# Kernel tuning notes

Measured on AMD Instinct MI355X. Metric: run time of the kernel, lower is better.

## Reference

```python
import jax, jax.numpy as jnp
import numpy as np

S, D = 16384, 1024


def setup_inputs() -> dict:
    key = jax.random.key(0)
    ks = jax.random.split(key, 7)
    stdv = 1.0 / np.sqrt(D)
    u = lambda k, shape: jax.random.uniform(k, shape, jnp.float32, -stdv, stdv)
    return {
        "x": jax.random.normal(ks[0], (S, D), jnp.float32),
        "Wq": u(ks[1], (D, D)), "bq": u(ks[2], (D,)),
        "Wk": u(ks[3], (D, D)), "bk": u(ks[4], (D,)),
        "Wv": u(ks[5], (D, D)), "bv": u(ks[6], (D,)),
    }


def reference(x, Wq, bq, Wk, bk, Wv, bv):
    # torch.nn.Linear: y = x @ W^T + b
    q = x @ Wq.T + bq          # [S, D]
    k = x @ Wk.T + bk          # [S, D]
    v = x @ Wv.T + bv          # [S, D]
    d = x.shape[-1]
    # NOTE: faithful to source -- scores are over the FEATURE axis: [D, D]
    scores = jnp.einsum('sd,se->de', q, k) / jnp.sqrt(jnp.float32(d))
    attn = jax.nn.softmax(scores, axis=-1)   # [D, D]
    out = v @ attn                           # [S, D]
    return out, attn
```

## Files before the change

kernel.cpp:

```cpp
#include <hip/hip_runtime.h>
#include <hip/hip_bf16.h>
#include <stdint.h>


#define S_ 16384
#define D_ 1024

typedef _Float16 half8 __attribute__((ext_vector_type(8)));
typedef _Float16 half4 __attribute__((ext_vector_type(4)));
typedef float f32x4 __attribute__((ext_vector_type(4)));

__device__ __forceinline__ void gload_lds16(const _Float16* g, _Float16* l) {
    __builtin_amdgcn_global_load_lds(
        (const __attribute__((address_space(1))) void*)g,
        (__attribute__((address_space(3))) void*)l, 16, 0, 0);
}

#define VM8() do { asm volatile("s_waitcnt vmcnt(8)" ::: "memory"); __builtin_amdgcn_sched_barrier(0); } while (0)
#define VM0() do { asm volatile("s_waitcnt vmcnt(0)" ::: "memory"); __builtin_amdgcn_sched_barrier(0); } while (0)
#define BAR() __builtin_amdgcn_s_barrier()
#define LGKM0() do { asm volatile("s_waitcnt lgkmcnt(0)" ::: "memory"); __builtin_amdgcn_sched_barrier(0); } while (0)
#define LGKM8() do { asm volatile("s_waitcnt lgkmcnt(8)" ::: "memory"); __builtin_amdgcn_sched_barrier(0); } while (0)
#define PRIO1() __builtin_amdgcn_s_setprio(1)
#define PRIO0() __builtin_amdgcn_s_setprio(0)

#define STAGEA(H, KT, NX) do { \
    const _Float16* _s = srcA + (size_t)((H) * 128) * lda + (size_t)(KT) * 64; \
    _Float16* _d = AsS + (NX) * 16384 + ((H) * 128 + 8 * w) * 64; \
    gload_lds16(_s, _d); \
    gload_lds16(_s + (size_t)64 * lda, _d + 4096); \
} while (0)

#define STAGEB(H, KT, NX) do { \
    const _Float16* _s = srcB + (size_t)((H) * 128) * ldb + (size_t)(KT) * 64; \
    _Float16* _d = BsS + (NX) * 16384 + ((H) * 128 + 8 * w) * 64; \
    gload_lds16(_s, _d); \
    gload_lds16(_s + (size_t)64 * ldb, _d + 4096); \
} while (0)

#define READA(PA, QA) do { _Pragma("unroll") \
    for (int fm = 0; fm < 4; ++fm) { \
        af[fm][0] = *(const half8*)((PA) + (((QA) * 128 + fm * 16) << 7) + cx0); \
        af[fm][1] = *(const half8*)((PA) + (((QA) * 128 + fm * 16) << 7) + cx1); } \
} while (0)

#define READB(PB, BF, QB) do { _Pragma("unroll") \
    for (int fn = 0; fn < 2; ++fn) { \
        BF[fn][0] = *(const half8*)((PB) + (((QB) * 128 + fn * 16) << 7) + cx0); \
        BF[fn][1] = *(const half8*)((PB) + (((QB) * 128 + fn * 16) << 7) + cx1); } \
} while (0)

#define MFMAB(QA, QB, BF) do { _Pragma("unroll") \
    for (int fm = 0; fm < 4; ++fm) { _Pragma("unroll") \
        for (int fn = 0; fn < 2; ++fn) { \
            f32x4 _c = acc[(QA) * 4 + fm][(QB) * 2 + fn]; \
            _c = __builtin_amdgcn_mfma_f32_16x16x32_f16(af[fm][0], BF[fn][0], _c, 0, 0, 0); \
            _c = __builtin_amdgcn_mfma_f32_16x16x32_f16(af[fm][1], BF[fn][1], _c, 0, 0, 0); \
            acc[(QA) * 4 + fm][(QB) * 2 + fn] = _c; } } \
} while (0)

__global__ __launch_bounds__(512, 2)
void gemm256(const _Float16* __restrict__ A, const _Float16* __restrict__ B,
             _Float16* __restrict__ C,
             int lda, int ldb, int ldc, int ksub, long long mn,
             int ntx, int ntxy, int cpx) {
    __shared__ _Float16 SM2[65536];
    _Float16* AsS = SM2;
    _Float16* BsS = SM2 + 32768;
    const int t = threadIdx.x;
    const int l = t & 63;
    const int w = t >> 6;
    const int wm = w >> 2, wn = w & 3;

    const int hb = blockIdx.x;
    const int lg = (hb & 7) * cpx + (hb >> 3);
    const int bz = lg / ntxy;
    const int rem = lg - bz * ntxy;
    const int by = rem / ntx;
    const int bx = rem - by * ntx;
    const size_t m0 = (size_t)by * 256;
    const size_t n0 = (size_t)bx * 256;
    const size_t k0 = (size_t)bz * (size_t)ksub;
    const long long coff = (long long)bz * mn;

    const int colsw = 8 * ((l & 7) ^ (l >> 3));
    const _Float16* srcA = A + (m0 + 8 * w + (l >> 3)) * (size_t)lda + k0 + colsw;
    const _Float16* srcB = B + (n0 + 8 * w + (l >> 3)) * (size_t)ldb + k0 + colsw;

    const int cx0 = (((l >> 4) << 4)) ^ ((l & 7) << 4);
    const int cx1 = (64 + ((l >> 4) << 4)) ^ ((l & 7) << 4);
    const char* basePA = (const char*)AsS + ((wm * 64 + (l & 15)) << 7);
    const char* basePB = (const char*)BsS + ((wn * 32 + (l & 15)) << 7);

    f32x4 acc[8][4] = {};
    half8 af[4][2], bf0[2][2], bf1[2][2];

    const int nk = ksub >> 6;

    STAGEA(0, 0, 0); STAGEB(0, 0, 0); STAGEB(1, 0, 0); STAGEA(1, 0, 0);
    STAGEA(0, 1, 1); STAGEB(0, 1, 1); STAGEB(1, 1, 1); STAGEA(1, 1, 1);

    for (int kt = 0; kt < nk; ++kt) {
        const int p = kt & 1;
        const int ks = kt + 2;
        const bool hs = ks < nk;
        const char* pA = basePA + p * 32768;
        const char* pB = basePB + p * 32768;

        if (kt == nk - 1) VM0(); else VM8();
        BAR();

        READA(pA, 0); READB(pB, bf0, 0);
        LGKM8();
        BAR(); LGKM0();
        PRIO1(); MFMAB(0, 0, bf0); PRIO0(); BAR();

        READB(pB, bf1, 1);
        if (hs) { STAGEA(0, ks, p); STAGEB(0, ks, p); }
        BAR(); LGKM0();
        PRIO1(); MFMAB(0, 1, bf1); PRIO0(); BAR();

        READA(pA, 1);
        if (hs) STAGEB(1, ks, p);
        BAR(); LGKM0();
        PRIO1(); MFMAB(1, 1, bf1); PRIO0(); BAR();

        if (hs) STAGEA(1, ks, p);
        PRIO1(); MFMAB(1, 0, bf0); PRIO0(); BAR();
    }

    _Float16* eb = SM2;
    const int cr = (l >> 4) << 2;
    const int cc = l & 15;
#pragma unroll
    for (int h = 0; h < 2; ++h) {
        BAR();
#pragma unroll
        for (int mm = 0; mm < 4; ++mm) {
#pragma unroll
            for (int n = 0; n < 4; ++n) {
                const int lrow0 = wm * 64 + mm * 16 + cr;
                const int lcol = (n >> 1) * 128 + wn * 32 + (n & 1) * 16 + cc;
#pragma unroll
                for (int r = 0; r < 4; ++r)
                    eb[(lrow0 + r) * 264 + lcol] = (_Float16)acc[h * 4 + mm][n][r];
            }
        }
        LGKM0();
        BAR();
#pragma unroll
        for (int i = 0; i < 8; ++i) {
            const int lrow = w * 16 + i * 2 + (l >> 5);
            const half8 v = *(const half8*)(eb + lrow * 264 + (l & 31) * 8);
            const size_t row = m0 + (size_t)h * 128 + lrow;
            const size_t col = n0 + (l & 31) * 8;
            __builtin_nontemporal_store(v,
                (half8*)(C + coff + (long long)row * ldc + col));
        }
        LGKM0();
    }
}

#define STG128(SRC, LD, DST, KT) do { \
    const _Float16* _s = (SRC) + (size_t)(KT) * 64; \
    _Float16* _d = (DST) + 8 * w * 64; \
    gload_lds16(_s, _d); \
    gload_lds16(_s + (size_t)32 * (LD), _d + 2048); \
    gload_lds16(_s + (size_t)64 * (LD), _d + 4096); \
    gload_lds16(_s + (size_t)96 * (LD), _d + 6144); \
} while (0)

__global__ __launch_bounds__(256, 2)
void gemm128(const _Float16* __restrict__ A, const _Float16* __restrict__ B,
             float* __restrict__ C, const float* __restrict__ bias,
             int lda, int ldb, int ldc, int ksub,
             int ntx, int cpx) {
    __shared__ _Float16 SM[32768];
    const int t = threadIdx.x;
    const int l = t & 63;
    const int w = t >> 6;
    const int wm = w >> 1, wn = w & 1;

    const int hb = blockIdx.x;
    const int lg = (hb & 7) * cpx + (hb >> 3);
    const int by = lg / ntx;
    const int bx = lg - by * ntx;
    const size_t m0 = (size_t)by * 128;
    const size_t n0 = (size_t)bx * 128;

    const int colsw = 8 * ((l & 7) ^ (l >> 3));
    const _Float16* srcA = A + (m0 + 8 * w + (l >> 3)) * (size_t)lda + colsw;
    const _Float16* srcB = B + (n0 + 8 * w + (l >> 3)) * (size_t)ldb + colsw;

    const int cx0 = (((l >> 4) << 4)) ^ ((l & 7) << 4);
    const int cx1 = (64 + ((l >> 4) << 4)) ^ ((l & 7) << 4);
    const char* basePA = (const char*)SM + ((wm * 64 + (l & 15)) << 7);
    const char* basePB = (const char*)SM + 32768 + ((wn * 64 + (l & 15)) << 7);

    f32x4 acc[4][4] = {};
    half8 af[4][2], bf[4][2];

    const int nk = ksub >> 6;

    STG128(srcA, lda, SM + 0, 0);        STG128(srcB, ldb, SM + 16384, 0);
    STG128(srcA, lda, SM + 8192, 1);     STG128(srcB, ldb, SM + 24576, 1);

    for (int kt = 0; kt < nk; ++kt) {
        const int p = kt & 1;
        const int ks = kt + 2;
        const bool hs = ks < nk;
        const char* pA = basePA + p * 16384;
        const char* pB = basePB + p * 16384;

        if (kt == nk - 1) VM0(); else VM8();
        BAR();

#pragma unroll
        for (int fm = 0; fm < 4; ++fm) {
            af[fm][0] = *(const half8*)(pA + ((fm * 16) << 7) + cx0);
            af[fm][1] = *(const half8*)(pA + ((fm * 16) << 7) + cx1);
        }
#pragma unroll
        for (int fn = 0; fn < 4; ++fn) {
            bf[fn][0] = *(const half8*)(pB + ((fn * 16) << 7) + cx0);
            bf[fn][1] = *(const half8*)(pB + ((fn * 16) << 7) + cx1);
        }
        LGKM0();
        PRIO1();
#pragma unroll
        for (int fm = 0; fm < 4; ++fm)
#pragma unroll
            for (int fn = 0; fn < 4; ++fn)
                acc[fm][fn] = __builtin_amdgcn_mfma_f32_16x16x32_f16(af[fm][0], bf[fn][0], acc[fm][fn], 0, 0, 0);
        PRIO0();
        BAR();

        if (hs) {
            STG128(srcA, lda, SM + p * 8192, ks);
            STG128(srcB, ldb, SM + 16384 + p * 8192, ks);
        }
        PRIO1();
#pragma unroll
        for (int fm = 0; fm < 4; ++fm)
#pragma unroll
            for (int fn = 0; fn < 4; ++fn)
                acc[fm][fn] = __builtin_amdgcn_mfma_f32_16x16x32_f16(af[fm][1], bf[fn][1], acc[fm][fn], 0, 0, 0);
        PRIO0();
        BAR();
    }

    float* lw = (float*)((char*)SM + w * 16384);
    const int cr = (l >> 4) << 2;
    const int cc = l & 15;
    float bb4[4];
#pragma unroll
    for (int fn = 0; fn < 4; ++fn)
        bb4[fn] = bias[n0 + wn * 64 + fn * 16 + cc];
#pragma unroll
    for (int h = 0; h < 2; ++h) {
#pragma unroll
        for (int mm2 = 0; mm2 < 2; ++mm2) {
            const int mm = h * 2 + mm2;
#pragma unroll
            for (int fn = 0; fn < 4; ++fn) {
                const int lcol = fn * 16 + cc;
                const int lrow = mm2 * 16 + cr;
#pragma unroll
                for (int r = 0; r < 4; ++r)
                    lw[(lrow + r) * 68 + lcol] = acc[mm][fn][r] + bb4[fn];
            }
        }
        LGKM0();
        const size_t grow0 = m0 + (size_t)wm * 64 + h * 32;
#pragma unroll
        for (int i = 0; i < 8; ++i) {
            const int lrow = i * 4 + (l >> 4);
            const int lcol = (l & 15) * 4;
            const f32x4 v = *(const f32x4*)(lw + lrow * 68 + lcol);
            __builtin_nontemporal_store(v,
                (f32x4*)(C + (size_t)(grow0 + lrow) * ldc + n0 + wn * 64 + lcol));
        }
        LGKM0();
    }
}

__global__ __launch_bounds__(256, 2)
void gemm_s128(const _Float16* __restrict__ A, const _Float16* __restrict__ B,
               float* __restrict__ C, int lda, int ldb, int ldc, int ksub,
               long long mn) {
    __shared__ _Float16 SM[32768];
    const int t = threadIdx.x;
    const int l = t & 63;
    const int w = t >> 6;
    const int wm = w >> 1, wn = w & 1;

    const size_t m0 = (size_t)blockIdx.y * 128;
    const size_t n0 = (size_t)blockIdx.x * 128;
    const size_t k0 = (size_t)blockIdx.z * (size_t)ksub;
    const long long coff = (long long)blockIdx.z * mn;

    const int colsw = 8 * ((l & 7) ^ (l >> 3));
    const _Float16* srcA = A + (m0 + 8 * w + (l >> 3)) * (size_t)lda + k0 + colsw;
    const _Float16* srcB = B + (n0 + 8 * w + (l >> 3)) * (size_t)ldb + k0 + colsw;

    const int cx0 = (((l >> 4) << 4)) ^ ((l & 7) << 4);
    const int cx1 = (64 + ((l >> 4) << 4)) ^ ((l & 7) << 4);
    const char* basePA = (const char*)SM + ((wm * 64 + (l & 15)) << 7);
    const char* basePB = (const char*)SM + 32768 + ((wn * 64 + (l & 15)) << 7);

    f32x4 acc[4][4] = {};
    half8 af[4][2], bf[4][2];

    const int nk = ksub >> 6;

    STG128(srcA, lda, SM + 0, 0);        STG128(srcB, ldb, SM + 16384, 0);
    STG128(srcA, lda, SM + 8192, 1);     STG128(srcB, ldb, SM + 24576, 1);

    for (int kt = 0; kt < nk; ++kt) {
        const int p = kt & 1;
        const int ks = kt + 2;
        const bool hs = ks < nk;
        const char* pA = basePA + p * 16384;
        const char* pB = basePB + p * 16384;

        if (kt == nk - 1) VM0(); else VM8();
        BAR();

#pragma unroll
        for (int fm = 0; fm < 4; ++fm) {
            af[fm][0] = *(const half8*)(pA + ((fm * 16) << 7) + cx0);
            af[fm][1] = *(const half8*)(pA + ((fm * 16) << 7) + cx1);
        }
#pragma unroll
        for (int fn = 0; fn < 4; ++fn) {
            bf[fn][0] = *(const half8*)(pB + ((fn * 16) << 7) + cx0);
            bf[fn][1] = *(const half8*)(pB + ((fn * 16) << 7) + cx1);
        }
        LGKM0();
        PRIO1();
#pragma unroll
        for (int fm = 0; fm < 4; ++fm)
#pragma unroll
            for (int fn = 0; fn < 4; ++fn)
                acc[fm][fn] = __builtin_amdgcn_mfma_f32_16x16x32_f16(af[fm][0], bf[fn][0], acc[fm][fn], 0, 0, 0);
        PRIO0();
        BAR();

        if (hs) {
            STG128(srcA, lda, SM + p * 8192, ks);
            STG128(srcB, ldb, SM + 16384 + p * 8192, ks);
        }
        PRIO1();
#pragma unroll
        for (int fm = 0; fm < 4; ++fm)
#pragma unroll
            for (int fn = 0; fn < 4; ++fn)
                acc[fm][fn] = __builtin_amdgcn_mfma_f32_16x16x32_f16(af[fm][1], bf[fn][1], acc[fm][fn], 0, 0, 0);
        PRIO0();
        BAR();
    }

    float* lw = (float*)((char*)SM + w * 16384);
    const int cr = (l >> 4) << 2;
    const int cc = l & 15;
#pragma unroll
    for (int h = 0; h < 2; ++h) {
#pragma unroll
        for (int mm2 = 0; mm2 < 2; ++mm2) {
            const int mm = h * 2 + mm2;
#pragma unroll
            for (int fn = 0; fn < 4; ++fn) {
                const int lcol = fn * 16 + cc;
                const int lrow = mm2 * 16 + cr;
#pragma unroll
                for (int r = 0; r < 4; ++r)
                    lw[(lrow + r) * 68 + lcol] = acc[mm][fn][r];
            }
        }
        LGKM0();
        const size_t grow0 = m0 + (size_t)wm * 64 + h * 32;
#pragma unroll
        for (int i = 0; i < 8; ++i) {
            const int lrow = i * 4 + (l >> 4);
            const int lcol = (l & 15) * 4;
            const f32x4 v = *(const f32x4*)(lw + lrow * 68 + lcol);
            *(f32x4*)(C + coff + (long long)(grow0 + lrow) * ldc + n0 + wn * 64 + lcol) = v;
        }
        LGKM0();
    }
}

template <int WRITE_ROW, int COLSUM>
__global__ __launch_bounds__(256)
void cast_transpose(const float* __restrict__ in, _Float16* __restrict__ outRow,
                    _Float16* __restrict__ outT, float* __restrict__ msum, int ldT) {
    __shared__ _Float16 tile[64][66];
    __shared__ float red[16][16][4];
    const int t = threadIdx.x;
    const int c0 = blockIdx.x * 64;
    const int r0 = blockIdx.y * 64;
    const int cg = t & 15;
    const int rb = t >> 4;
    f32x4 csum = {};
#pragma unroll
    for (int it = 0; it < 4; ++it) {
        const int rr = rb + it * 16;
        f32x4 v = *(const f32x4*)(in + (size_t)(r0 + rr) * 1024 + c0 + cg * 4);
        if (COLSUM) { csum[0] += v[0]; csum[1] += v[1]; csum[2] += v[2]; csum[3] += v[3]; }
        _Float16 h0 = (_Float16)v[0], h1 = (_Float16)v[1];
        _Float16 h2 = (_Float16)v[2], h3 = (_Float16)v[3];
        tile[rr][cg * 4 + 0] = h0; tile[rr][cg * 4 + 1] = h1;
        tile[rr][cg * 4 + 2] = h2; tile[rr][cg * 4 + 3] = h3;
        if (WRITE_ROW) {
            half4 h = {h0, h1, h2, h3};
            *(half4*)(outRow + (size_t)(r0 + rr) * 1024 + c0 + cg * 4) = h;
        }
    }
    if (COLSUM) {
        red[rb][cg][0] = csum[0]; red[rb][cg][1] = csum[1];
        red[rb][cg][2] = csum[2]; red[rb][cg][3] = csum[3];
    }
    __syncthreads();
    if (COLSUM && t < 64) {
        float s = 0.f;
#pragma unroll
        for (int k = 0; k < 16; ++k) s += red[k][t >> 2][t & 3];
        atomicAdd(msum + c0 + t, s);
    }
    const int i = t >> 2, ch = (t & 3) * 16;
    half8 h0v, h1v;
#pragma unroll
    for (int j = 0; j < 8; ++j) h0v[j] = tile[ch + j][i];
#pragma unroll
    for (int j = 0; j < 8; ++j) h1v[j] = tile[ch + 8 + j][i];
    *(half8*)(outT + (size_t)(c0 + i) * ldT + r0 + ch) = h0v;
    *(half8*)(outT + (size_t)(c0 + i) * ldT + r0 + ch + 8) = h1v;
}

__global__ __launch_bounds__(256)
void prep_w(const float* __restrict__ Wq, const float* __restrict__ Wk,
            const float* __restrict__ Wv, const float* __restrict__ bq,
            const float* __restrict__ m,
            _Float16* __restrict__ wq16, _Float16* __restrict__ wk16,
            _Float16* __restrict__ wvT16,
            float* __restrict__ u2, float* __restrict__ w) {
    __shared__ _Float16 tile[64][66];
    __shared__ float wred[4];
    const int b = blockIdx.x;
    const int t = threadIdx.x;

    if (b < 1024) {
        const bool isQ = b < 512;
        const int bb = isQ ? b : b - 512;
        const float* W = isQ ? Wq : Wk;
        _Float16* o = isQ ? wq16 : wk16;
        const size_t base = (size_t)bb * 2048 + (size_t)t * 8;
        const f32x4* p = (const f32x4*)(W + base);
        f32x4 x0 = p[0], x1 = p[1];
        half8 h;
        h[0] = (_Float16)x0[0]; h[1] = (_Float16)x0[1];
        h[2] = (_Float16)x0[2]; h[3] = (_Float16)x0[3];
        h[4] = (_Float16)x1[0]; h[5] = (_Float16)x1[1];
        h[6] = (_Float16)x1[2]; h[7] = (_Float16)x1[3];
        ((half8*)o)[bb * 256 + t] = h;
        const int col = (t * 8) & 1023;
        f32x4 m0 = *(const f32x4*)(m + col);
        f32x4 m1 = *(const f32x4*)(m + col + 4);
        float s = x0[0] * m0[0] + x0[1] * m0[1] + x0[2] * m0[2] + x0[3] * m0[3]
                + x1[0] * m1[0] + x1[1] * m1[1] + x1[2] * m1[2] + x1[3] * m1[3];
        for (int o2 = 32; o2; o2 >>= 1) s += __shfl_xor(s, o2);
        if ((t & 63) == 0) wred[t >> 6] = s;
        __syncthreads();
        if (t == 0) {
            const int rA = 2 * bb, rB = 2 * bb + 1;
            const float vA = wred[0] + wred[1];
            const float vB = wred[2] + wred[3];
            if (isQ) {
                u2[rA] = vA + 16384.0f * bq[rA];
                u2[rB] = vB + 16384.0f * bq[rB];
            } else {
                w[rA] = vA;
                w[rB] = vB;
            }
        }
        return;
    }

    const int bb = b - 1024;
    const int c0 = (bb & 15) * 64;
    const int r0 = (bb >> 4) * 64;
    const int cg = t & 15;
    const int rb = t >> 4;
#pragma unroll
    for (int it = 0; it < 4; ++it) {
        const int rr = rb + it * 16;
        f32x4 v = *(const f32x4*)(Wv + (size_t)(r0 + rr) * 1024 + c0 + cg * 4);
        tile[rr][cg * 4 + 0] = (_Float16)v[0];
        tile[rr][cg * 4 + 1] = (_Float16)v[1];
        tile[rr][cg * 4 + 2] = (_Float16)v[2];
        tile[rr][cg * 4 + 3] = (_Float16)v[3];
    }
    __syncthreads();
    const int i = t >> 2, ch = (t & 3) * 16;
    half8 h0v, h1v;
#pragma unroll
    for (int j = 0; j < 8; ++j) h0v[j] = tile[ch + j][i];
#pragma unroll
    for (int j = 0; j < 8; ++j) h1v[j] = tile[ch + 8 + j][i];
    *(half8*)(wvT16 + (size_t)(c0 + i) * 1024 + r0 + ch) = h0v;
    *(half8*)(wvT16 + (size_t)(c0 + i) * 1024 + r0 + ch + 8) = h1v;
}

__global__ void zero_vec(float* __restrict__ p, int n) {
    int i = blockIdx.x * 256 + threadIdx.x;
    if (i < n) p[i] = 0.f;
}

__global__ __launch_bounds__(256)
void reduce_g(const _Float16* __restrict__ part, _Float16* __restrict__ G16) {
    const size_t off = ((size_t)blockIdx.x * 256 + threadIdx.x) * 8;
    float s[8] = {};
    for (int z = 0; z < 16; ++z) {
        half8 v = *(const half8*)(part + (size_t)z * 1048576 + off);
#pragma unroll
        for (int j = 0; j < 8; ++j) s[j] += (float)v[j];
    }
    half8 o;
#pragma unroll
    for (int j = 0; j < 8; ++j) o[j] = (_Float16)s[j];
    *(half8*)(G16 + off) = o;
}

__global__ __launch_bounds__(256)
void reduce_cast(const float* __restrict__ part, _Float16* __restrict__ outh,
                 int nz, float scale) {
    const int idx = (blockIdx.x * 256 + threadIdx.x) * 4;
    f32x4 s = {};
    for (int z = 0; z < nz; ++z) {
        f32x4 v = *(const f32x4*)(part + (size_t)z * 1048576 + idx);
        s[0] += v[0]; s[1] += v[1]; s[2] += v[2]; s[3] += v[3];
    }
    half4 h;
    h[0] = (_Float16)(s[0] * scale); h[1] = (_Float16)(s[1] * scale);
    h[2] = (_Float16)(s[2] * scale); h[3] = (_Float16)(s[3] * scale);
    *(half4*)(outh + idx) = h;
}

__global__ __launch_bounds__(256)
void softmax_rows(const float* __restrict__ part, const float* __restrict__ u2,
                  const float* __restrict__ bq, const float* __restrict__ bk,
                  const float* __restrict__ w,
                  float* __restrict__ P, _Float16* __restrict__ PT) {
    const int a = blockIdx.x;
    const int t = threadIdx.x;
    __shared__ float red[8];
    const size_t off = (size_t)a * 1024 + t * 4;
    f32x4 s = {};
#pragma unroll
    for (int z = 0; z < 4; ++z) {
        f32x4 v = *(const f32x4*)(part + (size_t)z * 1048576 + off);
        s[0] += v[0]; s[1] += v[1]; s[2] += v[2]; s[3] += v[3];
    }
    const float ru = u2[a], rb = bq[a];
    f32x4 bk4 = *(const f32x4*)(bk + t * 4);
    f32x4 w4 = *(const f32x4*)(w + t * 4);
#pragma unroll
    for (int j = 0; j < 4; ++j) s[j] = (s[j] + ru * bk4[j] + rb * w4[j]) * 0.03125f;

    float m = fmaxf(fmaxf(s[0], s[1]), fmaxf(s[2], s[3]));
    for (int o = 32; o; o >>= 1) m = fmaxf(m, __shfl_xor(m, o));
    if ((t & 63) == 0) red[t >> 6] = m;
    __syncthreads();
    m = fmaxf(fmaxf(red[0], red[1]), fmaxf(red[2], red[3]));

    float e0 = expf(s[0] - m), e1 = expf(s[1] - m);
    float e2 = expf(s[2] - m), e3 = expf(s[3] - m);
    float sum = e0 + e1 + e2 + e3;
    for (int o = 32; o; o >>= 1) sum += __shfl_xor(sum, o);
    if ((t & 63) == 0) red[4 + (t >> 6)] = sum;
    __syncthreads();
    sum = red[4] + red[5] + red[6] + red[7];
    const float inv = 1.0f / sum;

    f32x4 o4 = {e0 * inv, e1 * inv, e2 * inv, e3 * inv};
    *(f32x4*)(P + off) = o4;
    const int b = t * 4;
    PT[(size_t)(b + 0) * 1024 + a] = (_Float16)o4[0];
    PT[(size_t)(b + 1) * 1024 + a] = (_Float16)o4[1];
    PT[(size_t)(b + 2) * 1024 + a] = (_Float16)o4[2];
    PT[(size_t)(b + 3) * 1024 + a] = (_Float16)o4[3];
}

__global__ __launch_bounds__(256)
void attn_bv(const float* __restrict__ attn, const float* __restrict__ bv,
             float* __restrict__ c) {
    const int j = blockIdx.x * 256 + threadIdx.x;
    const int a0 = blockIdx.y * 64;
    float s = 0.f;
#pragma unroll 4
    for (int k = 0; k < 64; ++k) {
        const int a = a0 + k;
        s += attn[(size_t)a * 1024 + j] * bv[a];
    }
    atomicAdd(c + j, s);
}

extern "C" void kernel_launch(void* const* d_in, const int* in_sizes, int n_in,
                              void* d_out, int out_size, void* d_ws, size_t ws_size,
                              hipStream_t stream) {
    const float* x  = (const float*)d_in[0];
    const float* Wq = (const float*)d_in[1];
    const float* bq = (const float*)d_in[2];
    const float* Wk = (const float*)d_in[3];
    const float* bk = (const float*)d_in[4];
    const float* Wv = (const float*)d_in[5];
    const float* bv = (const float*)d_in[6];
    float* out  = (float*)d_out;
    float* attn = out + (size_t)S_ * D_;

    char* ws = (char*)d_ws;
    float*    part  = (float*)ws;
    _Float16* partH = (_Float16*)ws;
    _Float16* x16   = (_Float16*)(ws + 33554432);
    _Float16* xT16  = (_Float16*)(ws + 67108864);
    _Float16* wq16  = (_Float16*)(ws + 100663296);
    _Float16* wk16  = (_Float16*)(ws + 102760448);
    _Float16* wvT16 = (_Float16*)(ws + 104857600);
    _Float16* G16   = (_Float16*)(ws + 106954752);
    _Float16* U16   = (_Float16*)(ws + 109051904);
    _Float16* PT    = (_Float16*)(ws + 111149056);
    _Float16* MT16  = (_Float16*)(ws + 113246208);
    float*    mvec  = (float*)(ws + 115343360);
    float*    u2    = mvec + 1024;
    float*    wv    = u2 + 1024;
    float*    cvec  = wv + 1024;

    zero_vec<<<16, 256, 0, stream>>>(mvec, 4096);
    cast_transpose<1, 1><<<dim3(16, 256), 256, 0, stream>>>(x, x16, xT16, mvec, S_);
    prep_w<<<1280, 256, 0, stream>>>(Wq, Wk, Wv, bq, mvec,
                                     wq16, wk16, wvT16, u2, wv);

    gemm256<<<256, 512, 0, stream>>>(xT16, xT16, partH,
                                     16384, 16384, 1024, 1024, 1048576LL,
                                     4, 16, 32);
    reduce_g<<<512, 256, 0, stream>>>(partH, G16);
    gemm_s128<<<dim3(8, 8, 4), 256, 0, stream>>>(wq16, G16, part,
                                                 1024, 1024, 1024, 256, 1048576);
    reduce_cast<<<1024, 256, 0, stream>>>(part, U16, 4, 1.0f);
    gemm_s128<<<dim3(8, 8, 4), 256, 0, stream>>>(U16, wk16, part,
                                                 1024, 1024, 1024, 256, 1048576);
    softmax_rows<<<1024, 256, 0, stream>>>(part, u2, bq, bk, wv, attn, PT);
    attn_bv<<<dim3(4, 16), 256, 0, stream>>>(attn, bv, cvec);
    gemm_s128<<<dim3(8, 8, 4), 256, 0, stream>>>(PT, wvT16, part,
                                                 1024, 1024, 1024, 256, 1048576);
    reduce_cast<<<1024, 256, 0, stream>>>(part, MT16, 4, 1.0f);
    gemm128<<<1024, 256, 0, stream>>>(x16, MT16, out, cvec,
                                      1024, 1024, 1024, 1024, 8, 128);
}
```

Baseline: 177.2 us.

## Replace 256-tile Gram GEMM with 128-tile split-K kernel and fp16 partials

The dedicated 256x256 gemm256 kernel for the Gram matrix xT·x is removed. That product now runs on the 128-tile split-K gemm_s128 with 8 K-splits of 2048, which gives 512 blocks instead of 256. gemm_s128 gains a template flag that writes fp16 partials through an LDS-staged epilogue, so two of the small GEMMs write half-precision partials and share a generic fp16 reduction instead of fp32 reduce_cast. This cuts partial-buffer traffic and improves occupancy, but it loses the larger tile's data reuse and rounds each partial sum to fp16.

```diff
diff --git a/kernel.cpp b/kernel.cpp
--- a/kernel.cpp
+++ b/kernel.cpp
@@ -20,146 +20,8 @@
 #define VM0() do { asm volatile("s_waitcnt vmcnt(0)" ::: "memory"); __builtin_amdgcn_sched_barrier(0); } while (0)
 #define BAR() __builtin_amdgcn_s_barrier()
 #define LGKM0() do { asm volatile("s_waitcnt lgkmcnt(0)" ::: "memory"); __builtin_amdgcn_sched_barrier(0); } while (0)
-#define LGKM8() do { asm volatile("s_waitcnt lgkmcnt(8)" ::: "memory"); __builtin_amdgcn_sched_barrier(0); } while (0)
 #define PRIO1() __builtin_amdgcn_s_setprio(1)
 #define PRIO0() __builtin_amdgcn_s_setprio(0)
-
-#define STAGEA(H, KT, NX) do { \
-    const _Float16* _s = srcA + (size_t)((H) * 128) * lda + (size_t)(KT) * 64; \
-    _Float16* _d = AsS + (NX) * 16384 + ((H) * 128 + 8 * w) * 64; \
-    gload_lds16(_s, _d); \
-    gload_lds16(_s + (size_t)64 * lda, _d + 4096); \
-} while (0)
-
-#define STAGEB(H, KT, NX) do { \
-    const _Float16* _s = srcB + (size_t)((H) * 128) * ldb + (size_t)(KT) * 64; \
-    _Float16* _d = BsS + (NX) * 16384 + ((H) * 128 + 8 * w) * 64; \
-    gload_lds16(_s, _d); \
-    gload_lds16(_s + (size_t)64 * ldb, _d + 4096); \
-} while (0)
-
-#define READA(PA, QA) do { _Pragma("unroll") \
-    for (int fm = 0; fm < 4; ++fm) { \
-        af[fm][0] = *(const half8*)((PA) + (((QA) * 128 + fm * 16) << 7) + cx0); \
-        af[fm][1] = *(const half8*)((PA) + (((QA) * 128 + fm * 16) << 7) + cx1); } \
-} while (0)
-
-#define READB(PB, BF, QB) do { _Pragma("unroll") \
-    for (int fn = 0; fn < 2; ++fn) { \
-        BF[fn][0] = *(const half8*)((PB) + (((QB) * 128 + fn * 16) << 7) + cx0); \
-        BF[fn][1] = *(const half8*)((PB) + (((QB) * 128 + fn * 16) << 7) + cx1); } \
-} while (0)
-
-#define MFMAB(QA, QB, BF) do { _Pragma("unroll") \
-    for (int fm = 0; fm < 4; ++fm) { _Pragma("unroll") \
-        for (int fn = 0; fn < 2; ++fn) { \
-            f32x4 _c = acc[(QA) * 4 + fm][(QB) * 2 + fn]; \
-            _c = __builtin_amdgcn_mfma_f32_16x16x32_f16(af[fm][0], BF[fn][0], _c, 0, 0, 0); \
-            _c = __builtin_amdgcn_mfma_f32_16x16x32_f16(af[fm][1], BF[fn][1], _c, 0, 0, 0); \
-            acc[(QA) * 4 + fm][(QB) * 2 + fn] = _c; } } \
-} while (0)
-
-__global__ __launch_bounds__(512, 2)
-void gemm256(const _Float16* __restrict__ A, const _Float16* __restrict__ B,
-             _Float16* __restrict__ C,
-             int lda, int ldb, int ldc, int ksub, long long mn,
-             int ntx, int ntxy, int cpx) {
-    __shared__ _Float16 SM2[65536];
-    _Float16* AsS = SM2;
-    _Float16* BsS = SM2 + 32768;
-    const int t = threadIdx.x;
-    const int l = t & 63;
-    const int w = t >> 6;
-    const int wm = w >> 2, wn = w & 3;
-
-    const int hb = blockIdx.x;
-    const int lg = (hb & 7) * cpx + (hb >> 3);
-    const int bz = lg / ntxy;
-    const int rem = lg - bz * ntxy;
-    const int by = rem / ntx;
-    const int bx = rem - by * ntx;
-    const size_t m0 = (size_t)by * 256;
-    const size_t n0 = (size_t)bx * 256;
-    const size_t k0 = (size_t)bz * (size_t)ksub;
-    const long long coff = (long long)bz * mn;
-
-    const int colsw = 8 * ((l & 7) ^ (l >> 3));
-    const _Float16* srcA = A + (m0 + 8 * w + (l >> 3)) * (size_t)lda + k0 + colsw;
-    const _Float16* srcB = B + (n0 + 8 * w + (l >> 3)) * (size_t)ldb + k0 + colsw;
-
-    const int cx0 = (((l >> 4) << 4)) ^ ((l & 7) << 4);
-    const int cx1 = (64 + ((l >> 4) << 4)) ^ ((l & 7) << 4);
-    const char* basePA = (const char*)AsS + ((wm * 64 + (l & 15)) << 7);
-    const char* basePB = (const char*)BsS + ((wn * 32 + (l & 15)) << 7);
-
-    f32x4 acc[8][4] = {};
-    half8 af[4][2], bf0[2][2], bf1[2][2];
-
-    const int nk = ksub >> 6;
-
-    STAGEA(0, 0, 0); STAGEB(0, 0, 0); STAGEB(1, 0, 0); STAGEA(1, 0, 0);
-    STAGEA(0, 1, 1); STAGEB(0, 1, 1); STAGEB(1, 1, 1); STAGEA(1, 1, 1);
-
-    for (int kt = 0; kt < nk; ++kt) {
-        const int p = kt & 1;
-        const int ks = kt + 2;
-        const bool hs = ks < nk;
-        const char* pA = basePA + p * 32768;
-        const char* pB = basePB + p * 32768;
-
-        if (kt == nk - 1) VM0(); else VM8();
-        BAR();
-
-        READA(pA, 0); READB(pB, bf0, 0);
-        LGKM8();
-        BAR(); LGKM0();
-        PRIO1(); MFMAB(0, 0, bf0); PRIO0(); BAR();
-
-        READB(pB, bf1, 1);
-        if (hs) { STAGEA(0, ks, p); STAGEB(0, ks, p); }
-        BAR(); LGKM0();
-        PRIO1(); MFMAB(0, 1, bf1); PRIO0(); BAR();
-
-        READA(pA, 1);
-        if (hs) STAGEB(1, ks, p);
-        BAR(); LGKM0();
-        PRIO1(); MFMAB(1, 1, bf1); PRIO0(); BAR();
-
-        if (hs) STAGEA(1, ks, p);
-        PRIO1(); MFMAB(1, 0, bf0); PRIO0(); BAR();
-    }
-
-    _Float16* eb = SM2;
-    const int cr = (l >> 4) << 2;
-    const int cc = l & 15;
-#pragma unroll
-    for (int h = 0; h < 2; ++h) {
-        BAR();
-#pragma unroll
-        for (int mm = 0; mm < 4; ++mm) {
-#pragma unroll
-            for (int n = 0; n < 4; ++n) {
-                const int lrow0 = wm * 64 + mm * 16 + cr;
-                const int lcol = (n >> 1) * 128 + wn * 32 + (n & 1) * 16 + cc;
-#pragma unroll
-                for (int r = 0; r < 4; ++r)
-                    eb[(lrow0 + r) * 264 + lcol] = (_Float16)acc[h * 4 + mm][n][r];
-            }
-        }
-        LGKM0();
-        BAR();
-#pragma unroll
-        for (int i = 0; i < 8; ++i) {
-            const int lrow = w * 16 + i * 2 + (l >> 5);
-            const half8 v = *(const half8*)(eb + lrow * 264 + (l & 31) * 8);
-            const size_t row = m0 + (size_t)h * 128 + lrow;
-            const size_t col = n0 + (l & 31) * 8;
-            __builtin_nontemporal_store(v,
-                (half8*)(C + coff + (long long)row * ldc + col));
-        }
-        LGKM0();
-    }
-}
 
 #define STG128(SRC, LD, DST, KT) do { \
     const _Float16* _s = (SRC) + (size_t)(KT) * 64; \
@@ -284,9 +146,10 @@
     }
 }
 
+template <int F16OUT>
 __global__ __launch_bounds__(256, 2)
 void gemm_s128(const _Float16* __restrict__ A, const _Float16* __restrict__ B,
-               float* __restrict__ C, int lda, int ldb, int ldc, int ksub,
+               void* __restrict__ C, int lda, int ldb, int ldc, int ksub,
                long long mn) {
     __shared__ _Float16 SM[32768];
     const int t = threadIdx.x;
@@ -360,33 +223,60 @@
         BAR();
     }
 
-    float* lw = (float*)((char*)SM + w * 16384);
     const int cr = (l >> 4) << 2;
     const int cc = l & 15;
-#pragma unroll
-    for (int h = 0; h < 2; ++h) {
-#pragma unroll
-        for (int mm2 = 0; mm2 < 2; ++mm2) {
-            const int mm = h * 2 + mm2;
+
+    if (F16OUT) {
+        _Float16* eb = SM;
+#pragma unroll
+        for (int fm = 0; fm < 4; ++fm) {
 #pragma unroll
             for (int fn = 0; fn < 4; ++fn) {
-                const int lcol = fn * 16 + cc;
-                const int lrow = mm2 * 16 + cr;
+                const int lrow0 = wm * 64 + fm * 16 + cr;
+                const int lcol = wn * 64 + fn * 16 + cc;
 #pragma unroll
                 for (int r = 0; r < 4; ++r)
-                    lw[(lrow + r) * 68 + lcol] = acc[mm][fn][r];
+                    eb[(lrow0 + r) * 132 + lcol] = (_Float16)acc[fm][fn][r];
             }
         }
         LGKM0();
-        const size_t grow0 = m0 + (size_t)wm * 64 + h * 32;
+        BAR();
+        _Float16* Ch = (_Float16*)C;
 #pragma unroll
         for (int i = 0; i < 8; ++i) {
-            const int lrow = i * 4 + (l >> 4);
-            const int lcol = (l & 15) * 4;
-            const f32x4 v = *(const f32x4*)(lw + lrow * 68 + lcol);
-            *(f32x4*)(C + coff + (long long)(grow0 + lrow) * ldc + n0 + wn * 64 + lcol) = v;
-        }
-        LGKM0();
+            const int row = i * 16 + (t >> 4);
+            const int colh = (t & 15) * 8;
+            const half8 v = *(const half8*)(eb + row * 132 + colh);
+            *(half8*)(Ch + coff + (long long)(m0 + row) * ldc + n0 + colh) = v;
+        }
+    } else {
+        float* lw = (float*)((char*)SM + w * 16384);
+        float* Cf = (float*)C;
+#pragma unroll
+        for (int h = 0; h < 2; ++h) {
+#pragma unroll
+            for (int mm2 = 0; mm2 < 2; ++mm2) {
+                const int mm = h * 2 + mm2;
+#pragma unroll
+                for (int fn = 0; fn < 4; ++fn) {
+                    const int lcol = fn * 16 + cc;
+                    const int lrow = mm2 * 16 + cr;
+#pragma unroll
+                    for (int r = 0; r < 4; ++r)
+                        lw[(lrow + r) * 68 + lcol] = acc[mm][fn][r];
+                }
+            }
+            LGKM0();
+            const size_t grow0 = m0 + (size_t)wm * 64 + h * 32;
+#pragma unroll
+            for (int i = 0; i < 8; ++i) {
+                const int lrow = i * 4 + (l >> 4);
+                const int lcol = (l & 15) * 4;
+                const f32x4 v = *(const f32x4*)(lw + lrow * 68 + lcol);
+                *(f32x4*)(Cf + coff + (long long)(grow0 + lrow) * ldc + n0 + wn * 64 + lcol) = v;
+            }
+            LGKM0();
+        }
     }
 }
 
@@ -517,10 +407,11 @@
 }
 
 __global__ __launch_bounds__(256)
-void reduce_g(const _Float16* __restrict__ part, _Float16* __restrict__ G16) {
+void reduce_h(const _Float16* __restrict__ part, _Float16* __restrict__ outh,
+              int nz) {
     const size_t off = ((size_t)blockIdx.x * 256 + threadIdx.x) * 8;
     float s[8] = {};
-    for (int z = 0; z < 16; ++z) {
+    for (int z = 0; z < nz; ++z) {
         half8 v = *(const half8*)(part + (size_t)z * 1048576 + off);
 #pragma unroll
         for (int j = 0; j < 8; ++j) s[j] += (float)v[j];
@@ -528,22 +419,7 @@
     half8 o;
 #pragma unroll
     for (int j = 0; j < 8; ++j) o[j] = (_Float16)s[j];
-    *(half8*)(G16 + off) = o;
-}
-
-__global__ __launch_bounds__(256)
-void reduce_cast(const float* __restrict__ part, _Float16* __restrict__ outh,
-                 int nz, float scale) {
-    const int idx = (blockIdx.x * 256 + threadIdx.x) * 4;
-    f32x4 s = {};
-    for (int z = 0; z < nz; ++z) {
-        f32x4 v = *(const f32x4*)(part + (size_t)z * 1048576 + idx);
-        s[0] += v[0]; s[1] += v[1]; s[2] += v[2]; s[3] += v[3];
-    }
-    half4 h;
-    h[0] = (_Float16)(s[0] * scale); h[1] = (_Float16)(s[1] * scale);
-    h[2] = (_Float16)(s[2] * scale); h[3] = (_Float16)(s[3] * scale);
-    *(half4*)(outh + idx) = h;
+    *(half8*)(outh + off) = o;
 }
 
 __global__ __launch_bounds__(256)
@@ -640,20 +516,19 @@
     prep_w<<<1280, 256, 0, stream>>>(Wq, Wk, Wv, bq, mvec,
                                      wq16, wk16, wvT16, u2, wv);
 
-    gemm256<<<256, 512, 0, stream>>>(xT16, xT16, partH,
-                                     16384, 16384, 1024, 1024, 1048576LL,
-                                     4, 16, 32);
-    reduce_g<<<512, 256, 0, stream>>>(partH, G16);
-    gemm_s128<<<dim3(8, 8, 4), 256, 0, stream>>>(wq16, G16, part,
-                                                 1024, 1024, 1024, 256, 1048576);
-    reduce_cast<<<1024, 256, 0, stream>>>(part, U16, 4, 1.0f);
-    gemm_s128<<<dim3(8, 8, 4), 256, 0, stream>>>(U16, wk16, part,
-                                                 1024, 1024, 1024, 256, 1048576);
+    gemm_s128<1><<<dim3(8, 8, 8), 256, 0, stream>>>(xT16, xT16, (void*)partH,
+                                                    16384, 16384, 1024, 2048, 1048576);
+    reduce_h<<<512, 256, 0, stream>>>(partH, G16, 8);
+    gemm_s128<1><<<dim3(8, 8, 4), 256, 0, stream>>>(wq16, G16, (void*)partH,
+                                                    1024, 1024, 1024, 256, 1048576);
+    reduce_h<<<512, 256, 0, stream>>>(partH, U16, 4);
+    gemm_s128<0><<<dim3(8, 8, 4), 256, 0, stream>>>(U16, wk16, (void*)part,
+                                                    1024, 1024, 1024, 256, 1048576);
     softmax_rows<<<1024, 256, 0, stream>>>(part, u2, bq, bk, wv, attn, PT);
     attn_bv<<<dim3(4, 16), 256, 0, stream>>>(attn, bv, cvec);
-    gemm_s128<<<dim3(8, 8, 4), 256, 0, stream>>>(PT, wvT16, part,
-                                                 1024, 1024, 1024, 256, 1048576);
-    reduce_cast<<<1024, 256, 0, stream>>>(part, MT16, 4, 1.0f);
+    gemm_s128<1><<<dim3(8, 8, 4), 256, 0, stream>>>(PT, wvT16, (void*)partH,
+                                                    1024, 1024, 1024, 256, 1048576);
+    reduce_h<<<512, 256, 0, stream>>>(partH, MT16, 4);
     gemm128<<<1024, 256, 0, stream>>>(x16, MT16, out, cvec,
                                       1024, 1024, 1024, 1024, 8, 128);
 }
```

Result: no change. 178.9 us (+0.9%).

## Exploit Gram matrix symmetry and write fp16 split-K partials

Applied to the files above, without the earlier changes.

The x^T x Gram GEMM now computes only the 10 upper-triangular 256x256 tile pairs instead of all 16, cutting its launch from 256 to 160 blocks. A mirror kernel then copies the missing lower tiles by transposing them. Two of the split-K small GEMMs now write fp16 partials instead of fp32, which halves the partial-sum traffic into the reduce kernels. The costs are an extra kernel launch for the mirror step and some precision loss from fp16 partial sums.

```diff
diff --git a/kernel.cpp b/kernel.cpp
--- a/kernel.cpp
+++ b/kernel.cpp
@@ -24,18 +24,25 @@
 #define PRIO1() __builtin_amdgcn_s_setprio(1)
 #define PRIO0() __builtin_amdgcn_s_setprio(0)
 
+#define PAIR10(PI, BY, BX) do { \
+    if ((PI) < 4) { BY = 0; BX = (PI); } \
+    else if ((PI) < 7) { BY = 1; BX = (PI) - 3; } \
+    else if ((PI) < 9) { BY = 2; BX = (PI) - 5; } \
+    else { BY = 3; BX = 3; } \
+} while (0)
+
 #define STAGEA(H, KT, NX) do { \
-    const _Float16* _s = srcA + (size_t)((H) * 128) * lda + (size_t)(KT) * 64; \
+    const _Float16* _s = srcA + (size_t)((H) * 128) * 16384 + (size_t)(KT) * 64; \
     _Float16* _d = AsS + (NX) * 16384 + ((H) * 128 + 8 * w) * 64; \
     gload_lds16(_s, _d); \
-    gload_lds16(_s + (size_t)64 * lda, _d + 4096); \
+    gload_lds16(_s + (size_t)64 * 16384, _d + 4096); \
 } while (0)
 
 #define STAGEB(H, KT, NX) do { \
-    const _Float16* _s = srcB + (size_t)((H) * 128) * ldb + (size_t)(KT) * 64; \
+    const _Float16* _s = srcB + (size_t)((H) * 128) * 16384 + (size_t)(KT) * 64; \
     _Float16* _d = BsS + (NX) * 16384 + ((H) * 128 + 8 * w) * 64; \
     gload_lds16(_s, _d); \
-    gload_lds16(_s + (size_t)64 * ldb, _d + 4096); \
+    gload_lds16(_s + (size_t)64 * 16384, _d + 4096); \
 } while (0)
 
 #define READA(PA, QA) do { _Pragma("unroll") \
@@ -60,10 +67,7 @@
 } while (0)
 
 __global__ __launch_bounds__(512, 2)
-void gemm256(const _Float16* __restrict__ A, const _Float16* __restrict__ B,
-             _Float16* __restrict__ C,
-             int lda, int ldb, int ldc, int ksub, long long mn,
-             int ntx, int ntxy, int cpx) {
+void gemm256G(const _Float16* __restrict__ A, _Float16* __restrict__ C) {
     __shared__ _Float16 SM2[65536];
     _Float16* AsS = SM2;
     _Float16* BsS = SM2 + 32768;
@@ -73,19 +77,19 @@
     const int wm = w >> 2, wn = w & 3;
 
     const int hb = blockIdx.x;
-    const int lg = (hb & 7) * cpx + (hb >> 3);
-    const int bz = lg / ntxy;
-    const int rem = lg - bz * ntxy;
-    const int by = rem / ntx;
-    const int bx = rem - by * ntx;
+    const int lg = (hb & 7) * 20 + (hb >> 3);
+    const int bz = lg / 10;
+    const int pi = lg - bz * 10;
+    int by, bx;
+    PAIR10(pi, by, bx);
     const size_t m0 = (size_t)by * 256;
     const size_t n0 = (size_t)bx * 256;
-    const size_t k0 = (size_t)bz * (size_t)ksub;
-    const long long coff = (long long)bz * mn;
+    const size_t k0 = (size_t)bz * 1024;
+    const long long coff = (long long)bz * 1048576LL;
 
     const int colsw = 8 * ((l & 7) ^ (l >> 3));
-    const _Float16* srcA = A + (m0 + 8 * w + (l >> 3)) * (size_t)lda + k0 + colsw;
-    const _Float16* srcB = B + (n0 + 8 * w + (l >> 3)) * (size_t)ldb + k0 + colsw;
+    const _Float16* srcA = A + (m0 + 8 * w + (l >> 3)) * (size_t)16384 + k0 + colsw;
+    const _Float16* srcB = A + (n0 + 8 * w + (l >> 3)) * (size_t)16384 + k0 + colsw;
 
     const int cx0 = (((l >> 4) << 4)) ^ ((l & 7) << 4);
     const int cx1 = (64 + ((l >> 4) << 4)) ^ ((l & 7) << 4);
@@ -95,7 +99,7 @@
     f32x4 acc[8][4] = {};
     half8 af[4][2], bf0[2][2], bf1[2][2];
 
-    const int nk = ksub >> 6;
+    const int nk = 16;
 
     STAGEA(0, 0, 0); STAGEB(0, 0, 0); STAGEB(1, 0, 0); STAGEA(1, 0, 0);
     STAGEA(0, 1, 1); STAGEB(0, 1, 1); STAGEB(1, 1, 1); STAGEA(1, 1, 1);
@@ -155,10 +159,64 @@
             const size_t row = m0 + (size_t)h * 128 + lrow;
             const size_t col = n0 + (l & 31) * 8;
             __builtin_nontemporal_store(v,
-                (half8*)(C + coff + (long long)row * ldc + col));
+                (half8*)(C + coff + (long long)row * 1024 + col));
         }
         LGKM0();
     }
+}
+
+__global__ __launch_bounds__(256)
+void reduce_h_u(const _Float16* __restrict__ part, _Float16* __restrict__ G16) {
+    const int b = blockIdx.x;
+    const int ti = b >> 5;
+    int by, bx;
+    PAIR10(ti, by, bx);
+    const int e0 = (b & 31) * 2048 + threadIdx.x * 8;
+    const size_t row = (size_t)by * 256 + (e0 >> 8);
+    const size_t col = (size_t)bx * 256 + (e0 & 255);
+    const size_t off = row * 1024 + col;
+    float s[8] = {};
+    for (int z = 0; z < 16; ++z) {
+        half8 v = *(const half8*)(part + (size_t)z * 1048576 + off);
+#pragma unroll
+        for (int j = 0; j < 8; ++j) s[j] += (float)v[j];
+    }
+    half8 o;
+#pragma unroll
+    for (int j = 0; j < 8; ++j) o[j] = (_Float16)s[j];
+    *(half8*)(G16 + off) = o;
+}
+
+__global__ __launch_bounds__(256)
+void mirror_g(_Float16* __restrict__ G) {
+    __shared__ _Float16 tile[64][66];
+    const int p = blockIdx.y;
+    int by, bx;
+    if (p < 3) { by = 0; bx = p + 1; }
+    else if (p < 5) { by = 1; bx = p - 1; }
+    else { by = 2; bx = 3; }
+    const int sy = blockIdx.x >> 2, sx = blockIdx.x & 3;
+    const int r0 = by * 256 + sy * 64;
+    const int c0 = bx * 256 + sx * 64;
+    const int t = threadIdx.x;
+    const int cg = t & 15;
+    const int rb = t >> 4;
+#pragma unroll
+    for (int it = 0; it < 4; ++it) {
+        const int rr = rb + it * 16;
+        half4 v = *(const half4*)(G + (size_t)(r0 + rr) * 1024 + c0 + cg * 4);
+        tile[rr][cg * 4 + 0] = v[0]; tile[rr][cg * 4 + 1] = v[1];
+        tile[rr][cg * 4 + 2] = v[2]; tile[rr][cg * 4 + 3] = v[3];
+    }
+    __syncthreads();
+    const int i = t >> 2, ch = (t & 3) * 16;
+    half8 h0v, h1v;
+#pragma unroll
+    for (int j = 0; j < 8; ++j) h0v[j] = tile[ch + j][i];
+#pragma unroll
+    for (int j = 0; j < 8; ++j) h1v[j] = tile[ch + 8 + j][i];
+    *(half8*)(G + (size_t)(c0 + i) * 1024 + r0 + ch) = h0v;
+    *(half8*)(G + (size_t)(c0 + i) * 1024 + r0 + ch + 8) = h1v;
 }
 
 #define STG128(SRC, LD, DST, KT) do { \
@@ -284,9 +342,10 @@
     }
 }
 
+template <int F16OUT>
 __global__ __launch_bounds__(256, 2)
 void gemm_s128(const _Float16* __restrict__ A, const _Float16* __restrict__ B,
-               float* __restrict__ C, int lda, int ldb, int ldc, int ksub,
+               void* __restrict__ C, int lda, int ldb, int ldc, int ksub,
                long long mn) {
     __shared__ _Float16 SM[32768];
     const int t = threadIdx.x;
@@ -360,33 +419,60 @@
         BAR();
     }
 
-    float* lw = (float*)((char*)SM + w * 16384);
     const int cr = (l >> 4) << 2;
     const int cc = l & 15;
-#pragma unroll
-    for (int h = 0; h < 2; ++h) {
-#pragma unroll
-        for (int mm2 = 0; mm2 < 2; ++mm2) {
-            const int mm = h * 2 + mm2;
+
+    if (F16OUT) {
+        _Float16* eb = SM;
+#pragma unroll
+        for (int fm = 0; fm < 4; ++fm) {
 #pragma unroll
             for (int fn = 0; fn < 4; ++fn) {
-                const int lcol = fn * 16 + cc;
-                const int lrow = mm2 * 16 + cr;
+                const int lrow0 = wm * 64 + fm * 16 + cr;
+                const int lcol = wn * 64 + fn * 16 + cc;
 #pragma unroll
                 for (int r = 0; r < 4; ++r)
-                    lw[(lrow + r) * 68 + lcol] = acc[mm][fn][r];
+                    eb[(lrow0 + r) * 132 + lcol] = (_Float16)acc[fm][fn][r];
             }
         }
         LGKM0();
-        const size_t grow0 = m0 + (size_t)wm * 64 + h * 32;
+        BAR();
+        _Float16* Ch = (_Float16*)C;
 #pragma unroll
         for (int i = 0; i < 8; ++i) {
-            const int lrow = i * 4 + (l >> 4);
-            const int lcol = (l & 15) * 4;
-            const f32x4 v = *(const f32x4*)(lw + lrow * 68 + lcol);
-            *(f32x4*)(C + coff + (long long)(grow0 + lrow) * ldc + n0 + wn * 64 + lcol) = v;
-        }
-        LGKM0();
+            const int row = i * 16 + (t >> 4);
+            const int colh = (t & 15) * 8;
+            const half8 v = *(const half8*)(eb + row * 132 + colh);
+            *(half8*)(Ch + coff + (long long)(m0 + row) * ldc + n0 + colh) = v;
+        }
+    } else {
+        float* lw = (float*)((char*)SM + w * 16384);
+        float* Cf = (float*)C;
+#pragma unroll
+        for (int h = 0; h < 2; ++h) {
+#pragma unroll
+            for (int mm2 = 0; mm2 < 2; ++mm2) {
+                const int mm = h * 2 + mm2;
+#pragma unroll
+                for (int fn = 0; fn < 4; ++fn) {
+                    const int lcol = fn * 16 + cc;
+                    const int lrow = mm2 * 16 + cr;
+#pragma unroll
+                    for (int r = 0; r < 4; ++r)
+                        lw[(lrow + r) * 68 + lcol] = acc[mm][fn][r];
+                }
+            }
+            LGKM0();
+            const size_t grow0 = m0 + (size_t)wm * 64 + h * 32;
+#pragma unroll
+            for (int i = 0; i < 8; ++i) {
+                const int lrow = i * 4 + (l >> 4);
+                const int lcol = (l & 15) * 4;
+                const f32x4 v = *(const f32x4*)(lw + lrow * 68 + lcol);
+                *(f32x4*)(Cf + coff + (long long)(grow0 + lrow) * ldc + n0 + wn * 64 + lcol) = v;
+            }
+            LGKM0();
+        }
     }
 }
 
@@ -517,10 +603,11 @@
 }
 
 __global__ __launch_bounds__(256)
-void reduce_g(const _Float16* __restrict__ part, _Float16* __restrict__ G16) {
+void reduce_h(const _Float16* __restrict__ part, _Float16* __restrict__ outh,
+              int nz) {
     const size_t off = ((size_t)blockIdx.x * 256 + threadIdx.x) * 8;
     float s[8] = {};
-    for (int z = 0; z < 16; ++z) {
+    for (int z = 0; z < nz; ++z) {
         half8 v = *(const half8*)(part + (size_t)z * 1048576 + off);
 #pragma unroll
         for (int j = 0; j < 8; ++j) s[j] += (float)v[j];
@@ -528,22 +615,7 @@
     half8 o;
 #pragma unroll
     for (int j = 0; j < 8; ++j) o[j] = (_Float16)s[j];
-    *(half8*)(G16 + off) = o;
-}
-
-__global__ __launch_bounds__(256)
-void reduce_cast(const float* __restrict__ part, _Float16* __restrict__ outh,
-                 int nz, float scale) {
-    const int idx = (blockIdx.x * 256 + threadIdx.x) * 4;
-    f32x4 s = {};
-    for (int z = 0; z < nz; ++z) {
-        f32x4 v = *(const f32x4*)(part + (size_t)z * 1048576 + idx);
-        s[0] += v[0]; s[1] += v[1]; s[2] += v[2]; s[3] += v[3];
-    }
-    half4 h;
-    h[0] = (_Float16)(s[0] * scale); h[1] = (_Float16)(s[1] * scale);
-    h[2] = (_Float16)(s[2] * scale); h[3] = (_Float16)(s[3] * scale);
-    *(half4*)(outh + idx) = h;
+    *(half8*)(outh + off) = o;
 }
 
 __global__ __launch_bounds__(256)
@@ -640,20 +712,19 @@
     prep_w<<<1280, 256, 0, stream>>>(Wq, Wk, Wv, bq, mvec,
                                      wq16, wk16, wvT16, u2, wv);
 
-    gemm256<<<256, 512, 0, stream>>>(xT16, xT16, partH,
-                                     16384, 16384, 1024, 1024, 1048576LL,
-                                     4, 16, 32);
-    reduce_g<<<512, 256, 0, stream>>>(partH, G16);
-    gemm_s128<<<dim3(8, 8, 4), 256, 0, stream>>>(wq16, G16, part,
-                                                 1024, 1024, 1024, 256, 1048576);
-    reduce_cast<<<1024, 256, 0, stream>>>(part, U16, 4, 1.0f);
-    gemm_s128<<<dim3(8, 8, 4), 256, 0, stream>>>(U16, wk16, part,
-                                                 1024, 1024, 1024, 256, 1048576);
+    gemm256G<<<160, 512, 0, stream>>>(xT16, partH);
+    reduce_h_u<<<320, 256, 0, stream>>>(partH, G16);
+    mirror_g<<<dim3(16, 6), 256, 0, stream>>>(G16);
+    gemm_s128<1><<<dim3(8, 8, 4), 256, 0, stream>>>(wq16, G16, (void*)partH,
+                                                    1024, 1024, 1024, 256, 1048576);
+    reduce_h<<<512, 256, 0, stream>>>(partH, U16, 4);
+    gemm_s128<0><<<dim3(8, 8, 4), 256, 0, stream>>>(U16, wk16, (void*)part,
+                                                    1024, 1024, 1024, 256, 1048576);
     softmax_rows<<<1024, 256, 0, stream>>>(part, u2, bq, bk, wv, attn, PT);
     attn_bv<<<dim3(4, 16), 256, 0, stream>>>(attn, bv, cvec);
-    gemm_s128<<<dim3(8, 8, 4), 256, 0, stream>>>(PT, wvT16, part,
-                                                 1024, 1024, 1024, 256, 1048576);
-    reduce_cast<<<1024, 256, 0, stream>>>(part, MT16, 4, 1.0f);
+    gemm_s128<1><<<dim3(8, 8, 4), 256, 0, stream>>>(PT, wvT16, (void*)partH,
+                                                    1024, 1024, 1024, 256, 1048576);
+    reduce_h<<<512, 256, 0, stream>>>(partH, MT16, 4);
     gemm128<<<1024, 256, 0, stream>>>(x16, MT16, out, cvec,
                                       1024, 1024, 1024, 1024, 8, 128);
 }
```

Result: faster. 165.5 us (-6.6%).
